# Kernel tuning notes

Measured on AMD Instinct MI355X. Metric: run time of the kernel, lower is better.

Reference implementation:

```python
import jax, jax.numpy as jnp
import numpy as np

B, H, W, C = 4, 64, 64, 256
CK = C // 8  # f/g projection dim = 32


def setup_inputs() -> dict:
    key = jax.random.key(0)
    ks = jax.random.split(key, 4)
    x = jax.random.normal(ks[0], (B, H, W, C), dtype=jnp.float32)
    Wf = jax.random.normal(ks[1], (C, CK), dtype=jnp.float32) * (1.0 / np.sqrt(C))
    Wg = jax.random.normal(ks[2], (C, CK), dtype=jnp.float32) * (1.0 / np.sqrt(C))
    Wh = jax.random.normal(ks[3], (C, C), dtype=jnp.float32) * (1.0 / np.sqrt(C))
    bf = jnp.zeros((CK,), jnp.float32)
    bg = jnp.zeros((CK,), jnp.float32)
    bh = jnp.zeros((C,), jnp.float32)
    return {"x": x, "Wf": Wf, "bf": bf, "Wg": Wg, "bg": bg, "Wh": Wh, "bh": bh}


def reference(x, Wf, bf, Wg, bg, Wh, bh):
    b, h, w, c = x.shape
    n = h * w
    xf = x.reshape(b, n, c)  # 1x1 conv == per-pixel matmul
    f = xf @ Wf + bf         # [b, n, c/8]  (keys)
    g = xf @ Wg + bg         # [b, n, c/8]  (queries)
    hh = xf @ Wh + bh        # [b, n, c]    (values)
    # s[i,j] = g_i . f_j  (tf.matmul(g, f, transpose_b=True))
    s = jnp.einsum('bik,bjk->bij', g, f)
    beta = jax.nn.softmax(s, axis=-1)
    o = jnp.einsum('bij,bjc->bic', beta, hh)
    return x + o.reshape(b, h, w, c)
```

## Files before the change

kernel.cpp:

```cpp
#include <hip/hip_runtime.h>
#include <math.h>

#define CDIM 256
#define CKD  32
#define NPIX 4096
#define BATCH 4
#define NMACRO (NPIX / 64)

typedef __attribute__((ext_vector_type(8)))  short bf16x8;
typedef __attribute__((ext_vector_type(16))) float f32x16;

#if __has_builtin(__builtin_amdgcn_exp2f)
#define EXP2(x) __builtin_amdgcn_exp2f(x)
#else
#define EXP2(x) exp2f(x)
#endif

__device__ inline ushort f2bf(float x) {
    unsigned u = __float_as_uint(x);
    u += 0x7fffu + ((u >> 16) & 1u);
    return (ushort)(u >> 16);
}
__device__ inline unsigned cvtpk(float a, float b) {
    unsigned r;
    asm("v_cvt_pk_bf16_f32 %0, %1, %2" : "=v"(r) : "v"(a), "v"(b));
    return r;
}
__device__ inline void lane32swap(unsigned &a, unsigned &b) {
    asm("v_permlane32_swap_b32 %0, %1" : "+v"(a), "+v"(b));
}

#define LDS_ASYNC16(gptr, lptr) \
  __builtin_amdgcn_global_load_lds((const __attribute__((address_space(1))) void*)(gptr), \
                                   (__attribute__((address_space(3))) void*)(lptr), 16, 0, 0)

__global__ __launch_bounds__(256) void prep_kernel(
    const float* __restrict__ Wh, const float* __restrict__ Wf,
    const float* __restrict__ Wg, ushort* __restrict__ Wt)
{
    __shared__ float ls[64 * 65];
    const int tid = threadIdx.x;
    const int bid = blockIdx.x;

    if (bid < 16) {
        const int k0 = (bid & 3) * 64, c0 = (bid >> 2) * 64;
        #pragma unroll
        for (int i = 0; i < 16; ++i) {
            int r = i * 4 + (tid >> 6), c = tid & 63;
            ls[r * 65 + c] = Wh[(k0 + r) * 256 + c0 + c];
        }
        __syncthreads();
        #pragma unroll
        for (int i = 0; i < 16; ++i) {
            int cr = i * 4 + (tid >> 6), k = tid & 63;
            Wt[(c0 + cr) * 256 + k0 + k] = f2bf(ls[k * 65 + cr]);
        }
    } else {
        const float* W = (bid == 16) ? Wf : Wg;
        const int rbase = 256 + (bid - 16) * 32;
        #pragma unroll
        for (int kh2 = 0; kh2 < 2; ++kh2) {
            __syncthreads();
            #pragma unroll
            for (int i = 0; i < 16; ++i) {
                int flat = i * 256 + tid;
                int k = flat >> 5, c = flat & 31;
                ls[c * 129 + k] = W[(kh2 * 128 + k) * 32 + c];
            }
            __syncthreads();
            #pragma unroll
            for (int i = 0; i < 16; ++i) {
                int flat = i * 256 + tid;
                int c = flat >> 7, k = flat & 127;
                Wt[(rbase + c) * 256 + kh2 * 128 + k] = f2bf(ls[c * 129 + k]);
            }
        }
    }
}

__global__ __launch_bounds__(256) void proj_kernel(
    const float*  __restrict__ x,
    const ushort* __restrict__ Wt,
    const float*  __restrict__ bfp, const float* __restrict__ bgp,
    const float*  __restrict__ bhp,
    ushort* __restrict__ fo,
    ushort* __restrict__ go,
    ushort* __restrict__ glo,
    ushort* __restrict__ ht)
{
    __shared__ ushort wls[2][1280 * 8];
    __shared__ ushort xls[2][128 * 8];

    const int tid  = threadIdx.x;
    const int w    = tid >> 6;
    const int lane = tid & 63;
    const int hl   = lane >> 5;
    const int ln   = lane & 31;
    const int bid  = blockIdx.x;
    const long long px0 = (long long)bid * 32;
    const int b    = (int)(px0 >> 12);
    const int n0   = (int)(px0 & (NPIX - 1));
    const int kt   = n0 >> 6;
    const int koff = n0 & 63;

    const int sx_px = tid >> 3, sx_j = tid & 7;
    const int sx_o = sx_j >> 1, sx_h = sx_j & 1;
    const int sx_slot = sx_o * 32 + ((sx_px + 2 * sx_o) & 31);

    #pragma unroll
    for (int i = 0; i < 5; ++i) {
        int s = i * 256 + tid;
        int n = s >> 2, o = ((s & 3) - (n >> 1)) & 3;
        LDS_ASYNC16(Wt + n * 256 + o * 8, &wls[0][s * 8]);
    }
    {
        float4 v = *(const float4*)(x + (px0 + sx_px) * CDIM + sx_j * 4);
        uint2 p; p.x = cvtpk(v.x, v.y); p.y = cvtpk(v.z, v.w);
        *(uint2*)&xls[0][sx_slot * 8 + sx_h * 4] = p;
    }

    f32x16 acc0={0,0,0,0,0,0,0,0,0,0,0,0,0,0,0,0};
    f32x16 acc1={0,0,0,0,0,0,0,0,0,0,0,0,0,0,0,0};
    f32x16 accfg={0,0,0,0,0,0,0,0,0,0,0,0,0,0,0,0};

    for (int sl = 0; sl < 8; ++sl) {
        const int cur = sl & 1;
        __syncthreads();
        if (sl + 1 < 8) {
            const int nxt = cur ^ 1;
            #pragma unroll
            for (int i = 0; i < 5; ++i) {
                int s = i * 256 + tid;
                int n = s >> 2, o = ((s & 3) - (n >> 1)) & 3;
                LDS_ASYNC16(Wt + n * 256 + (sl + 1) * 32 + o * 8, &wls[nxt][s * 8]);
            }
            float4 v = *(const float4*)(x + (px0 + sx_px) * CDIM + (sl + 1) * 32 + sx_j * 4);
            uint2 p; p.x = cvtpk(v.x, v.y); p.y = cvtpk(v.z, v.w);
            *(uint2*)&xls[nxt][sx_slot * 8 + sx_h * 4] = p;
        }

        #pragma unroll
        for (int st = 0; st < 2; ++st) {
            const int o = st * 2 + hl;
            #define LDW(n) (*(const bf16x8*)&wls[cur][((n) * 4 + (((o) + ((n) >> 1)) & 3)) * 8])
            bf16x8 xb  = *(const bf16x8*)&xls[cur][(o * 32 + ((ln + 2 * o) & 31)) * 8];
            bf16x8 wa0 = LDW(w * 64 + ln);
            bf16x8 wa1 = LDW(w * 64 + 32 + ln);
            acc0 = __builtin_amdgcn_mfma_f32_32x32x16_bf16(wa0, xb, acc0, 0, 0, 0);
            acc1 = __builtin_amdgcn_mfma_f32_32x32x16_bf16(wa1, xb, acc1, 0, 0, 0);
            if (w < 2) {
                bf16x8 wfg = LDW(256 + w * 32 + ln);
                accfg = __builtin_amdgcn_mfma_f32_32x32x16_bf16(xb, wfg, accfg, 0, 0, 0);
            }
            #undef LDW
        }
    }

    ushort* htt = ht + ((long long)(b * 64 + kt) * CDIM) * 64 + koff;
    #pragma unroll
    for (int r = 0; r < 16; ++r) {
        const int rowD = (r & 3) + 8 * (r >> 2) + 4 * hl;
        int c0 = w * 64 + rowD, c1 = c0 + 32;
        htt[(long long)c0 * 64 + ln] = f2bf(acc0[r] + bhp[c0]);
        htt[(long long)c1 * 64 + ln] = f2bf(acc1[r] + bhp[c1]);
    }
    if (w < 2) {
        const float bb = (w ? bgp : bfp)[ln];
        const float scl = w ? 1.44269504088896f : 1.0f;
        #pragma unroll
        for (int r = 0; r < 16; ++r) {
            const int rowD = (r & 3) + 8 * (r >> 2) + 4 * hl;
            float v = (accfg[r] + bb) * scl;
            ushort hi = f2bf(v);
            long long idx = (px0 + rowD) * CKD + ln;
            if (w == 0) {
                fo[idx] = hi;
            } else {
                go[idx] = hi;
                float hif = __uint_as_float(((unsigned)hi) << 16);
                glo[idx] = f2bf(v - hif);
            }
        }
    }
}

__global__ __launch_bounds__(256, 2) void attn_kernel(
    const float*  __restrict__ x,
    const ushort* __restrict__ fk,
    const ushort* __restrict__ gq,
    const ushort* __restrict__ glo,
    const ushort* __restrict__ hv,
    float* __restrict__ out)
{
    __shared__ ushort hh_lds[2][1024 * 8];
    __shared__ ushort f_lds[2][256 * 8];
    __shared__ float  l_red[2][64];

    const int tid  = threadIdx.x;
    const int w    = tid >> 6;
    const int lane = tid & 63;
    const int hl   = lane >> 5;
    const int ln   = lane & 31;

    const int bid = blockIdx.x;
    const int chs = bid & 1;
    const int b   = (bid >> 1) & 3;
    const int qt  = bid >> 3;
    const int q0  = qt * 64;

    const int qb = w & 1;
    const int kh = w >> 1;

    const long long bbase = (long long)b * NPIX;
    const ushort* fbase = fk + bbase * CKD;
    const ushort* htb   = hv + (long long)b * 64 * (CDIM * 64);

    const ushort* gp  = gq  + (bbase + q0 + qb * 32 + ln) * CKD;
    const ushort* glp = glo + (bbase + q0 + qb * 32 + ln) * CKD;
    const bf16x8 ga0 = *(const bf16x8*)(gp + hl * 8);
    const bf16x8 ga1 = *(const bf16x8*)(gp + 16 + hl * 8);
    const bf16x8 gl0 = *(const bf16x8*)(glp + hl * 8);
    const bf16x8 gl1 = *(const bf16x8*)(glp + 16 + hl * 8);

    #pragma unroll
    for (int i = 0; i < 4; ++i) {
        int s = i * 256 + tid;
        int c = s >> 3, j = ((s & 7) - c) & 7;
        LDS_ASYNC16(htb + (long long)(chs * 128 + c) * 64 + j * 8, &hh_lds[0][s * 8]);
    }
    LDS_ASYNC16(fbase + (long long)(tid & 63) * CKD + (tid >> 6) * 8, &f_lds[0][tid * 8]);

    const f32x16 Zv = {0,0,0,0,0,0,0,0,0,0,0,0,0,0,0,0};
    f32x16 acc0={0,0,0,0,0,0,0,0,0,0,0,0,0,0,0,0};
    f32x16 acc1={0,0,0,0,0,0,0,0,0,0,0,0,0,0,0,0};
    f32x16 acc2={0,0,0,0,0,0,0,0,0,0,0,0,0,0,0,0};
    f32x16 acc3={0,0,0,0,0,0,0,0,0,0,0,0,0,0,0,0};
    float lsum = 0.f;

    #pragma unroll 2
    for (int kt = 0; kt < NMACRO; ++kt) {
        const int cur = kt & 1;
        __syncthreads();

        if (kt + 1 < NMACRO) {
            const int nxt = cur ^ 1;
            const long long tb = (long long)(kt + 1) * (CDIM * 64);
            #pragma unroll
            for (int i = 0; i < 4; ++i) {
                int s = i * 256 + tid;
                int c = s >> 3, j = ((s & 7) - c) & 7;
                LDS_ASYNC16(htb + tb + (long long)(chs * 128 + c) * 64 + j * 8,
                            &hh_lds[nxt][s * 8]);
            }
            LDS_ASYNC16(fbase + (long long)((kt + 1) * 64 + (tid & 63)) * CKD + (tid >> 6) * 8,
                        &f_lds[nxt][tid * 8]);
        }

        f32x16 S;
        {
            bf16x8 fb0 = *(const bf16x8*)&f_lds[cur][((hl)     * 64 + kh * 32 + ln) * 8];
            bf16x8 fb1 = *(const bf16x8*)&f_lds[cur][((2 + hl) * 64 + kh * 32 + ln) * 8];
            __builtin_amdgcn_s_setprio(1);
            S = __builtin_amdgcn_mfma_f32_32x32x16_bf16(fb0, ga0, Zv, 0, 0, 0);
            S = __builtin_amdgcn_mfma_f32_32x32x16_bf16(fb0, gl0, S, 0, 0, 0);
            S = __builtin_amdgcn_mfma_f32_32x32x16_bf16(fb1, ga1, S, 0, 0, 0);
            S = __builtin_amdgcn_mfma_f32_32x32x16_bf16(fb1, gl1, S, 0, 0, 0);
            __builtin_amdgcn_s_setprio(0);
        }

        float p[16];
        #pragma unroll
        for (int r = 0; r < 16; ++r) {
            p[r] = EXP2(fminf(S[r], 115.41f));
            lsum += p[r];
        }
        unsigned U[8];
        #pragma unroll
        for (int m = 0; m < 8; ++m) U[m] = cvtpk(p[2*m], p[2*m+1]);

        #pragma unroll
        for (int ck = 0; ck < 2; ++ck) {
            unsigned a0 = U[4*ck + 0], a1 = U[4*ck + 1];
            unsigned a2 = U[4*ck + 2], a3 = U[4*ck + 3];
            lane32swap(a0, a2);
            lane32swap(a1, a3);
            union { unsigned i[4]; bf16x8 v; } pf;
            pf.i[0] = a0; pf.i[1] = a1; pf.i[2] = a2; pf.i[3] = a3;
            bf16x8 pa = pf.v;
            const int oct = kh * 4 + ck * 2 + hl;
            const int c0 = ln, c1 = 32 + ln, c2 = 64 + ln, c3 = 96 + ln;
            bf16x8 hb0 = *(const bf16x8*)&hh_lds[cur][(c0 * 8 + ((oct + c0) & 7)) * 8];
            bf16x8 hb1 = *(const bf16x8*)&hh_lds[cur][(c1 * 8 + ((oct + c1) & 7)) * 8];
            bf16x8 hb2 = *(const bf16x8*)&hh_lds[cur][(c2 * 8 + ((oct + c2) & 7)) * 8];
            bf16x8 hb3 = *(const bf16x8*)&hh_lds[cur][(c3 * 8 + ((oct + c3) & 7)) * 8];
            __builtin_amdgcn_s_setprio(1);
            acc0 = __builtin_amdgcn_mfma_f32_32x32x16_bf16(pa, hb0, acc0, 0, 0, 0);
            acc1 = __builtin_amdgcn_mfma_f32_32x32x16_bf16(pa, hb1, acc1, 0, 0, 0);
            acc2 = __builtin_amdgcn_mfma_f32_32x32x16_bf16(pa, hb2, acc2, 0, 0, 0);
            acc3 = __builtin_amdgcn_mfma_f32_32x32x16_bf16(pa, hb3, acc3, 0, 0, 0);
            __builtin_amdgcn_s_setprio(0);
        }
    }

    lsum += __shfl_xor(lsum, 32);
    __syncthreads();
    if (hl == 0) l_red[kh][qb * 32 + ln] = lsum;
    float* O_s = (float*)hh_lds;
    if (kh == 0) {
        #pragma unroll
        for (int r = 0; r < 16; ++r) {
            int rowD = (r & 3) + 8 * (r >> 2) + 4 * hl;
            O_s[((qb * 4 + 2) * 32 + rowD) * 32 + ln] = acc2[r];
            O_s[((qb * 4 + 3) * 32 + rowD) * 32 + ln] = acc3[r];
        }
    } else {
        #pragma unroll
        for (int r = 0; r < 16; ++r) {
            int rowD = (r & 3) + 8 * (r >> 2) + 4 * hl;
            O_s[((qb * 4 + 0) * 32 + rowD) * 32 + ln] = acc0[r];
            O_s[((qb * 4 + 1) * 32 + rowD) * 32 + ln] = acc1[r];
        }
    }
    __syncthreads();

    if (kh == 0) {
        #pragma unroll
        for (int r = 0; r < 16; ++r) {
            int rowD = (r & 3) + 8 * (r >> 2) + 4 * hl;
            int ql = qb * 32 + rowD;
            float linv = 1.f / (l_red[0][ql] + l_red[1][ql]);
            long long rg = (bbase + q0 + ql) * CDIM + chs * 128 + ln;
            float o0 = acc0[r] + O_s[((qb * 4 + 0) * 32 + rowD) * 32 + ln];
            float o1 = acc1[r] + O_s[((qb * 4 + 1) * 32 + rowD) * 32 + ln];
            out[rg]      = x[rg]      + o0 * linv;
            out[rg + 32] = x[rg + 32] + o1 * linv;
        }
    } else {
        #pragma unroll
        for (int r = 0; r < 16; ++r) {
            int rowD = (r & 3) + 8 * (r >> 2) + 4 * hl;
            int ql = qb * 32 + rowD;
            float linv = 1.f / (l_red[0][ql] + l_red[1][ql]);
            long long rg = (bbase + q0 + ql) * CDIM + chs * 128 + 64 + ln;
            float o2 = acc2[r] + O_s[((qb * 4 + 2) * 32 + rowD) * 32 + ln];
            float o3 = acc3[r] + O_s[((qb * 4 + 3) * 32 + rowD) * 32 + ln];
            out[rg]      = x[rg]      + o2 * linv;
            out[rg + 32] = x[rg + 32] + o3 * linv;
        }
    }
}

extern "C" void kernel_launch(void* const* d_in, const int* in_sizes, int n_in,
                              void* d_out, int out_size, void* d_ws, size_t ws_size,
                              hipStream_t stream) {
    const float* x  = (const float*)d_in[0];
    const float* Wf = (const float*)d_in[1];
    const float* bf = (const float*)d_in[2];
    const float* Wg = (const float*)d_in[3];
    const float* bg = (const float*)d_in[4];
    const float* Wh = (const float*)d_in[5];
    const float* bh = (const float*)d_in[6];
    float* out = (float*)d_out;

    ushort* fbf = (ushort*)d_ws;
    ushort* gbf = fbf + BATCH * NPIX * CKD;
    ushort* glo = gbf + BATCH * NPIX * CKD;
    ushort* ht  = glo + BATCH * NPIX * CKD;
    ushort* Wt  = ht + BATCH * NPIX * CDIM;

    prep_kernel<<<dim3(18), 256, 0, stream>>>(Wh, Wf, Wg, Wt);
    proj_kernel<<<dim3(512), 256, 0, stream>>>(x, Wt, bf, bg, bh, fbf, gbf, glo, ht);
    attn_kernel<<<dim3(512), 256, 0, stream>>>(x, fbf, gbf, glo, ht, out);
}
```

Measured before the change: 162.3 us.

## Split attention over key ranges with partial outputs and a combine kernel

Adds a split-K scheme to the attention kernel: each query tile's keys are divided into three ranges, each handled by a separate block that writes unnormalized fp32 partial outputs and row sums to workspace. A new combine kernel sums the partials, normalizes, and adds the residual. Occupancy hint rises to 3 blocks per CU, the exp clamp is dropped, row-sum accumulation is split across two registers, and the x-to-bf16 conversion in the projection kernel switches from the hardware pack instruction to software rounding. The cost is about 50MB of extra fp32 partial traffic plus a fourth launch, and removing the clamp risks overflow because there is no running max.

Result: slower. 168.1 us (+3.6%).

```diff
diff --git a/kernel.cpp b/kernel.cpp
--- a/kernel.cpp
+++ b/kernel.cpp
@@ -20,6 +20,9 @@
     unsigned u = __float_as_uint(x);
     u += 0x7fffu + ((u >> 16) & 1u);
     return (ushort)(u >> 16);
+}
+__device__ inline unsigned packbf(float a, float b) {
+    return (unsigned)f2bf(a) | ((unsigned)f2bf(b) << 16);
 }
 __device__ inline unsigned cvtpk(float a, float b) {
     unsigned r;
@@ -115,7 +118,7 @@
     }
     {
         float4 v = *(const float4*)(x + (px0 + sx_px) * CDIM + sx_j * 4);
-        uint2 p; p.x = cvtpk(v.x, v.y); p.y = cvtpk(v.z, v.w);
+        uint2 p; p.x = packbf(v.x, v.y); p.y = packbf(v.z, v.w);
         *(uint2*)&xls[0][sx_slot * 8 + sx_h * 4] = p;
     }
 
@@ -135,7 +138,7 @@
                 LDS_ASYNC16(Wt + n * 256 + (sl + 1) * 32 + o * 8, &wls[nxt][s * 8]);
             }
             float4 v = *(const float4*)(x + (px0 + sx_px) * CDIM + (sl + 1) * 32 + sx_j * 4);
-            uint2 p; p.x = cvtpk(v.x, v.y); p.y = cvtpk(v.z, v.w);
+            uint2 p; p.x = packbf(v.x, v.y); p.y = packbf(v.z, v.w);
             *(uint2*)&xls[nxt][sx_slot * 8 + sx_h * 4] = p;
         }
 
@@ -184,13 +187,16 @@
     }
 }
 
-__global__ __launch_bounds__(256, 2) void attn_kernel(
+__global__ __launch_bounds__(256, 3) void attn_kernel(
     const float*  __restrict__ x,
     const ushort* __restrict__ fk,
     const ushort* __restrict__ gq,
     const ushort* __restrict__ glo,
     const ushort* __restrict__ hv,
-    float* __restrict__ out)
+    float* __restrict__ out,
+    float* __restrict__ Opart,
+    float* __restrict__ Lpart,
+    int nks)
 {
     __shared__ ushort hh_lds[2][1024 * 8];
     __shared__ ushort f_lds[2][256 * 8];
@@ -205,8 +211,13 @@
     const int bid = blockIdx.x;
     const int chs = bid & 1;
     const int b   = (bid >> 1) & 3;
-    const int qt  = bid >> 3;
+    const int rest = bid >> 3;
+    const int qt  = rest & 63;
+    const int ks  = rest >> 6;
     const int q0  = qt * 64;
+    const int kt0 = (ks * NMACRO) / nks;
+    const int kt1 = ((ks + 1) * NMACRO) / nks;
+    const int nmac = kt1 - kt0;
 
     const int qb = w & 1;
     const int kh = w >> 1;
@@ -222,27 +233,32 @@
     const bf16x8 gl0 = *(const bf16x8*)(glp + hl * 8);
     const bf16x8 gl1 = *(const bf16x8*)(glp + 16 + hl * 8);
 
-    #pragma unroll
-    for (int i = 0; i < 4; ++i) {
-        int s = i * 256 + tid;
-        int c = s >> 3, j = ((s & 7) - c) & 7;
-        LDS_ASYNC16(htb + (long long)(chs * 128 + c) * 64 + j * 8, &hh_lds[0][s * 8]);
-    }
-    LDS_ASYNC16(fbase + (long long)(tid & 63) * CKD + (tid >> 6) * 8, &f_lds[0][tid * 8]);
+    {
+        const long long tb = (long long)kt0 * (CDIM * 64);
+        #pragma unroll
+        for (int i = 0; i < 4; ++i) {
+            int s = i * 256 + tid;
+            int c = s >> 3, j = ((s & 7) - c) & 7;
+            LDS_ASYNC16(htb + tb + (long long)(chs * 128 + c) * 64 + j * 8, &hh_lds[0][s * 8]);
+        }
+        LDS_ASYNC16(fbase + (long long)(kt0 * 64 + (tid & 63)) * CKD + (tid >> 6) * 8,
+                    &f_lds[0][tid * 8]);
+    }
 
     const f32x16 Zv = {0,0,0,0,0,0,0,0,0,0,0,0,0,0,0,0};
     f32x16 acc0={0,0,0,0,0,0,0,0,0,0,0,0,0,0,0,0};
     f32x16 acc1={0,0,0,0,0,0,0,0,0,0,0,0,0,0,0,0};
     f32x16 acc2={0,0,0,0,0,0,0,0,0,0,0,0,0,0,0,0};
     f32x16 acc3={0,0,0,0,0,0,0,0,0,0,0,0,0,0,0,0};
-    float lsum = 0.f;
+    float lsA = 0.f, lsB = 0.f;
 
     #pragma unroll 2
-    for (int kt = 0; kt < NMACRO; ++kt) {
-        const int cur = kt & 1;
+    for (int m = 0; m < nmac; ++m) {
+        const int kt = kt0 + m;
+        const int cur = m & 1;
         __syncthreads();
 
-        if (kt + 1 < NMACRO) {
+        if (m + 1 < nmac) {
             const int nxt = cur ^ 1;
             const long long tb = (long long)(kt + 1) * (CDIM * 64);
             #pragma unroll
@@ -271,12 +287,12 @@
         float p[16];
         #pragma unroll
         for (int r = 0; r < 16; ++r) {
-            p[r] = EXP2(fminf(S[r], 115.41f));
-            lsum += p[r];
+            p[r] = EXP2(S[r]);
+            if (r & 1) lsB += p[r]; else lsA += p[r];
         }
         unsigned U[8];
         #pragma unroll
-        for (int m = 0; m < 8; ++m) U[m] = cvtpk(p[2*m], p[2*m+1]);
+        for (int m2 = 0; m2 < 8; ++m2) U[m2] = cvtpk(p[2*m2], p[2*m2+1]);
 
         #pragma unroll
         for (int ck = 0; ck < 2; ++ck) {
@@ -302,6 +318,7 @@
         }
     }
 
+    float lsum = lsA + lsB;
     lsum += __shfl_xor(lsum, 32);
     __syncthreads();
     if (hl == 0) l_red[kh][qb * 32 + ln] = lsum;
@@ -323,31 +340,85 @@
     }
     __syncthreads();
 
-    if (kh == 0) {
-        #pragma unroll
-        for (int r = 0; r < 16; ++r) {
-            int rowD = (r & 3) + 8 * (r >> 2) + 4 * hl;
-            int ql = qb * 32 + rowD;
-            float linv = 1.f / (l_red[0][ql] + l_red[1][ql]);
-            long long rg = (bbase + q0 + ql) * CDIM + chs * 128 + ln;
-            float o0 = acc0[r] + O_s[((qb * 4 + 0) * 32 + rowD) * 32 + ln];
-            float o1 = acc1[r] + O_s[((qb * 4 + 1) * 32 + rowD) * 32 + ln];
-            out[rg]      = x[rg]      + o0 * linv;
-            out[rg + 32] = x[rg + 32] + o1 * linv;
+    if (Opart) {
+        const long long pb = ((long long)(ks * BATCH + b) * NPIX + q0);
+        if (w == 0 && chs == 0)
+            Lpart[pb + lane] = l_red[0][lane] + l_red[1][lane];
+        if (kh == 0) {
+            #pragma unroll
+            for (int r = 0; r < 16; ++r) {
+                int rowD = (r & 3) + 8 * (r >> 2) + 4 * hl;
+                int ql = qb * 32 + rowD;
+                long long rg = (pb + ql) * CDIM + chs * 128 + ln;
+                Opart[rg]      = acc0[r] + O_s[((qb * 4 + 0) * 32 + rowD) * 32 + ln];
+                Opart[rg + 32] = acc1[r] + O_s[((qb * 4 + 1) * 32 + rowD) * 32 + ln];
+            }
+        } else {
+            #pragma unroll
+            for (int r = 0; r < 16; ++r) {
+                int rowD = (r & 3) + 8 * (r >> 2) + 4 * hl;
+                int ql = qb * 32 + rowD;
+                long long rg = (pb + ql) * CDIM + chs * 128 + 64 + ln;
+                Opart[rg]      = acc2[r] + O_s[((qb * 4 + 2) * 32 + rowD) * 32 + ln];
+                Opart[rg + 32] = acc3[r] + O_s[((qb * 4 + 3) * 32 + rowD) * 32 + ln];
+            }
         }
     } else {
-        #pragma unroll
-        for (int r = 0; r < 16; ++r) {
-            int rowD = (r & 3) + 8 * (r >> 2) + 4 * hl;
-            int ql = qb * 32 + rowD;
-            float linv = 1.f / (l_red[0][ql] + l_red[1][ql]);
-            long long rg = (bbase + q0 + ql) * CDIM + chs * 128 + 64 + ln;
-            float o2 = acc2[r] + O_s[((qb * 4 + 2) * 32 + rowD) * 32 + ln];
-            float o3 = acc3[r] + O_s[((qb * 4 + 3) * 32 + rowD) * 32 + ln];
-            out[rg]      = x[rg]      + o2 * linv;
-            out[rg + 32] = x[rg + 32] + o3 * linv;
-        }
-    }
+        if (kh == 0) {
+            #pragma unroll
+            for (int r = 0; r < 16; ++r) {
+                int rowD = (r & 3) + 8 * (r >> 2) + 4 * hl;
+                int ql = qb * 32 + rowD;
+                float linv = 1.f / (l_red[0][ql] + l_red[1][ql]);
+                long long rg = (bbase + q0 + ql) * CDIM + chs * 128 + ln;
+                float o0 = acc0[r] + O_s[((qb * 4 + 0) * 32 + rowD) * 32 + ln];
+                float o1 = acc1[r] + O_s[((qb * 4 + 1) * 32 + rowD) * 32 + ln];
+                out[rg]      = x[rg]      + o0 * linv;
+                out[rg + 32] = x[rg + 32] + o1 * linv;
+            }
+        } else {
+            #pragma unroll
+            for (int r = 0; r < 16; ++r) {
+                int rowD = (r & 3) + 8 * (r >> 2) + 4 * hl;
+                int ql = qb * 32 + rowD;
+                float linv = 1.f / (l_red[0][ql] + l_red[1][ql]);
+                long long rg = (bbase + q0 + ql) * CDIM + chs * 128 + 64 + ln;
+                float o2 = acc2[r] + O_s[((qb * 4 + 2) * 32 + rowD) * 32 + ln];
+                float o3 = acc3[r] + O_s[((qb * 4 + 3) * 32 + rowD) * 32 + ln];
+                out[rg]      = x[rg]      + o2 * linv;
+                out[rg + 32] = x[rg + 32] + o3 * linv;
+            }
+        }
+    }
+}
+
+__global__ __launch_bounds__(256) void combine_kernel(
+    const float* __restrict__ x, const float* __restrict__ Op,
+    const float* __restrict__ Lp, float* __restrict__ out, int nks)
+{
+    const int tid = threadIdx.x, w = tid >> 6, lane = tid & 63;
+    const int row = blockIdx.x * 4 + w;
+    const int b = row >> 12, q = row & (NPIX - 1);
+
+    float l = 0.f;
+    for (int ks = 0; ks < nks; ++ks)
+        l += Lp[(ks * BATCH + b) * NPIX + q];
+    const float linv = 1.f / l;
+
+    float4 a = {0.f, 0.f, 0.f, 0.f};
+    for (int ks = 0; ks < nks; ++ks) {
+        const float4 v = *(const float4*)&Op[
+            (((long long)(ks * BATCH + b) * NPIX + q)) * CDIM + lane * 4];
+        a.x += v.x; a.y += v.y; a.z += v.z; a.w += v.w;
+    }
+    const long long g = ((long long)b * NPIX + q) * CDIM + lane * 4;
+    const float4 xv = *(const float4*)&x[g];
+    float4 o;
+    o.x = xv.x + a.x * linv;
+    o.y = xv.y + a.y * linv;
+    o.z = xv.z + a.z * linv;
+    o.w = xv.w + a.w * linv;
+    *(float4*)&out[g] = o;
 }
 
 extern "C" void kernel_launch(void* const* d_in, const int* in_sizes, int n_in,
@@ -367,8 +438,25 @@
     ushort* glo = gbf + BATCH * NPIX * CKD;
     ushort* ht  = glo + BATCH * NPIX * CKD;
     ushort* Wt  = ht + BATCH * NPIX * CDIM;
+    char*   pb  = (char*)(Wt + 320 * 256);
+
+    const int NKS = 3;
+    const size_t base_used = (size_t)(pb - (char*)d_ws);
+    const size_t oelems = (size_t)NKS * BATCH * NPIX * CDIM;
+    const size_t lelems = (size_t)NKS * BATCH * NPIX;
+    float* Opart = nullptr;
+    float* Lpart = nullptr;
+    int nks = 1;
+    if (ws_size >= base_used + (oelems + lelems) * sizeof(float)) {
+        nks = NKS;
+        Opart = (float*)pb;
+        Lpart = Opart + oelems;
+    }
 
     prep_kernel<<<dim3(18), 256, 0, stream>>>(Wh, Wf, Wg, Wt);
     proj_kernel<<<dim3(512), 256, 0, stream>>>(x, Wt, bf, bg, bh, fbf, gbf, glo, ht);
-    attn_kernel<<<dim3(512), 256, 0, stream>>>(x, fbf, gbf, glo, ht, out);
-}
+    attn_kernel<<<dim3(512 * nks), 256, 0, stream>>>(x, fbf, gbf, glo, ht, out,
+                                                     Opart, Lpart, nks);
+    if (nks > 1)
+        combine_kernel<<<dim3(BATCH * NPIX / 4), 256, 0, stream>>>(x, Opart, Lpart, out, nks);
+}
```
